# Performance work log

Hardware: AMD Instinct MI355X
Metric: run time of the kernel (lower is better)

## Reference

```python
import jax, jax.numpy as jnp
import numpy as np

B, L, C, H = 2, 2048, 1024, 16  # batches, tokens per batch, channels, heads


def _ln(x, eps=1e-6):
    # LayerNorm32: no affine, eps=1e-6, computed in fp32
    x32 = x.astype(jnp.float32)
    m = x32.mean(-1, keepdims=True)
    v = ((x32 - m) ** 2).mean(-1, keepdims=True)
    return ((x32 - m) * jax.lax.rsqrt(v + eps)).astype(x.dtype)


def setup_inputs() -> dict:
    key = jax.random.key(0)
    ks = jax.random.split(key, 8)
    s = 0.02
    return {
        "feats": jax.random.normal(ks[0], (B * L, C), jnp.float32),
        "mod": jax.random.normal(ks[1], (B, C), jnp.float32),
        "w_mod": jax.random.normal(ks[2], (C, 6 * C), jnp.float32) * s,
        "b_mod": jnp.zeros((6 * C,), jnp.float32),
        "w_qkv": jax.random.normal(ks[3], (C, 3 * C), jnp.float32) * s,
        "b_qkv": jnp.zeros((3 * C,), jnp.float32),
        "w_proj": jax.random.normal(ks[4], (C, C), jnp.float32) * s,
        "b_proj": jnp.zeros((C,), jnp.float32),
        "w_fc1": jax.random.normal(ks[5], (C, 4 * C), jnp.float32) * s,
        "b_fc1": jnp.zeros((4 * C,), jnp.float32),
        "w_fc2": jax.random.normal(ks[6], (4 * C, C), jnp.float32) * s,
        "b_fc2": jnp.zeros((C,), jnp.float32),
        "seq_len": L,
    }


def reference(feats, mod, w_mod, b_mod, w_qkv, b_qkv, w_proj, b_proj,
              w_fc1, b_fc1, w_fc2, b_fc2, seq_len):
    Bn, Cn = mod.shape
    Ln = seq_len
    Hn = H
    D = Cn // Hn

    # adaLN modulation: SiLU -> Linear(C, 6C), chunk into 6 [B, C] pieces
    m = jax.nn.silu(mod) @ w_mod + b_mod
    sh_a, sc_a, g_a, sh_m, sc_m, g_m = jnp.split(m, 6, axis=1)

    x = feats.reshape(Bn, Ln, Cn)

    # --- MSA branch ---
    h = _ln(x)
    h = h * (1.0 + sc_a[:, None]) + sh_a[:, None]
    qkv = h @ w_qkv + b_qkv  # [B, L, 3C]
    q, k, v = [t.reshape(Bn, Ln, Hn, D) for t in jnp.split(qkv, 3, axis=-1)]
    scores = jnp.einsum('bqhd,bkhd->bhqk', q, k) / jnp.sqrt(jnp.float32(D))
    a = jax.nn.softmax(scores, axis=-1)
    o = jnp.einsum('bhqk,bkhd->bqhd', a, v).reshape(Bn, Ln, Cn)
    o = o @ w_proj + b_proj
    x = x + o * g_a[:, None]

    # --- FFN branch ---
    h = _ln(x)
    h = h * (1.0 + sc_m[:, None]) + sh_m[:, None]
    h = jax.nn.gelu(h @ w_fc1 + b_fc1, approximate=False) @ w_fc2 + b_fc2
    x = x + h * g_m[:, None]

    return x.reshape(Bn * Ln, Cn)
```

## Files before the change

### kernel.cpp

```cpp
#include <hip/hip_runtime.h>
#include <hip/hip_bf16.h>
#include <math.h>

#define B_ 2
#define L_ 2048
#define C_ 1024
#define H_ 16
#define D_ 64

typedef __attribute__((ext_vector_type(8))) short short8;
typedef __attribute__((ext_vector_type(4))) float float4v;

__device__ inline short f2bs(float f) {
    union { __hip_bfloat16 h; short s; } u; u.h = __float2bfloat16(f); return u.s;
}

#define GL2LDS(gp, lp)                                                         \
    __builtin_amdgcn_global_load_lds(                                          \
        (const __attribute__((address_space(1))) void*)(gp),                   \
        (__attribute__((address_space(3))) void*)(lp), 16, 0, 0)

__global__ __launch_bounds__(256) void k_mod2(const float* __restrict__ mod,
                                              const float* __restrict__ w_mod,
                                              const float* __restrict__ b_mod,
                                              float* __restrict__ m_out) {
    __shared__ float a_s[2][256];
    const int t = threadIdx.x;
    const int seg = blockIdx.y;
    for (int i = t; i < 512; i += 256) {
        float a = mod[(i >> 8) * C_ + seg * 256 + (i & 255)];
        a_s[i >> 8][i & 255] = a / (1.f + __expf(-a));
    }
    __syncthreads();
    int j = blockIdx.x * 256 + t;
    float acc0 = (seg == 0) ? b_mod[j] : 0.f;
    float acc1 = acc0;
    for (int k = 0; k < 256; ++k) {
        float w = w_mod[(size_t)(seg * 256 + k) * (6 * C_) + j];
        acc0 += a_s[0][k] * w;
        acc1 += a_s[1][k] * w;
    }
    atomicAdd(&m_out[j], acc0);
    atomicAdd(&m_out[6 * C_ + j], acc1);
}

__global__ __launch_bounds__(256) void k_wt_all(
        const float* __restrict__ w_qkv, const float* __restrict__ w_proj,
        const float* __restrict__ w_fc1, const float* __restrict__ w_fc2,
        short* __restrict__ wqkvT, short* __restrict__ wprojT,
        short* __restrict__ wfc1T, short* __restrict__ wfc2T) {
    __shared__ short T[64][72];
    int id = blockIdx.x;
    const float* W; short* WT; int K, N;
    if (id < 768)       {             W = w_qkv;  WT = wqkvT;  K = C_;     N = 3 * C_; }
    else if (id < 1024) { id -= 768;  W = w_proj; WT = wprojT; K = C_;     N = C_;     }
    else if (id < 2048) { id -= 1024; W = w_fc1;  WT = wfc1T;  K = C_;     N = 4 * C_; }
    else                { id -= 2048; W = w_fc2;  WT = wfc2T;  K = 4 * C_; N = C_;     }
    const int nb = N >> 6;
    const int n0 = (id % nb) * 64, k0 = (id / nb) * 64;
    const int t = threadIdx.x;
    {
        int kr = t >> 2, nc = (t & 3) * 16;
        const float* src = W + (size_t)(k0 + kr) * N + n0 + nc;
#pragma unroll
        for (int j = 0; j < 16; ++j) T[kr][nc + j] = f2bs(src[j]);
    }
    __syncthreads();
    {
        int nr = t >> 2, kc = (t & 3) * 16;
        short8 o0, o1;
#pragma unroll
        for (int j = 0; j < 8; ++j) { o0[j] = T[kc + j][nr]; o1[j] = T[kc + 8 + j][nr]; }
        short* dst = WT + (size_t)(n0 + nr) * K + k0 + kc;
        *(short8*)dst = o0;
        *(short8*)(dst + 8) = o1;
    }
}

__global__ __launch_bounds__(256) void k_vt(const __hip_bfloat16* __restrict__ qkv,
                                            short* __restrict__ vt) {
    __shared__ short T[64][72];
    const int t = threadIdx.x;
    const int kt = blockIdx.x * 64;
    const int bh = blockIdx.y;
    const int h = bh & (H_ - 1), b = bh >> 4;
    const __hip_bfloat16* src = qkv + ((size_t)(b * L_ + kt)) * (3 * C_) + 2 * C_ + h * D_;
    {
        int kr = t >> 2, dg = (t & 3) * 16;
        const short8* s = (const short8*)(src + (size_t)kr * (3 * C_) + dg);
        *(short8*)&T[kr][dg] = s[0];
        *(short8*)&T[kr][dg + 8] = s[1];
    }
    __syncthreads();
    {
        int dr = t >> 2, kg = (t & 3) * 16;
        short8 o0, o1;
#pragma unroll
        for (int j = 0; j < 8; ++j) { o0[j] = T[kg + j][dr]; o1[j] = T[kg + 8 + j][dr]; }
        short* dst = vt + ((size_t)bh * D_ + dr) * L_ + kt + kg;
        *(short8*)dst = o0;
        *(short8*)(dst + 8) = o1;
    }
}

__global__ __launch_bounds__(256) void k_ln_mod(const float* __restrict__ x,
                                                const float* __restrict__ mvec,
                                                int off_sh, int off_sc,
                                                __hip_bfloat16* __restrict__ h_out) {
    int row = blockIdx.x;
    int b = row / L_;
    int t = threadIdx.x;
    float v[4];
    float s = 0.f, ss = 0.f;
#pragma unroll
    for (int i = 0; i < 4; ++i) {
        int c = t + i * 256;
        float val = x[(size_t)row * C_ + c];
        v[i] = val; s += val; ss += val * val;
    }
#pragma unroll
    for (int o = 32; o; o >>= 1) { s += __shfl_xor(s, o); ss += __shfl_xor(ss, o); }
    __shared__ float red[2][4];
    int wid = t >> 6, lane = t & 63;
    if (lane == 0) { red[0][wid] = s; red[1][wid] = ss; }
    __syncthreads();
    s  = red[0][0] + red[0][1] + red[0][2] + red[0][3];
    ss = red[1][0] + red[1][1] + red[1][2] + red[1][3];
    float mean = s * (1.f / C_);
    float var  = ss * (1.f / C_) - mean * mean;
    float rstd = rsqrtf(var + 1e-6f);
#pragma unroll
    for (int i = 0; i < 4; ++i) {
        int c = t + i * 256;
        float sc = mvec[b * (6 * C_) + off_sc + c];
        float sh = mvec[b * (6 * C_) + off_sh + c];
        float hn = (v[i] - mean) * rstd;
        h_out[(size_t)row * C_ + c] = __float2bfloat16(hn * (1.f + sc) + sh);
    }
}

__device__ inline void gemm_epilogue(float v, int m, int n, int N, int act, int emode,
                                     const float* __restrict__ gate,
                                     const float* __restrict__ resid_f,
                                     __hip_bfloat16* __restrict__ out_bf,
                                     float* __restrict__ out_f) {
    if (act == 1) v = 0.5f * v * (1.f + erff(v * 0.70710678118654752440f));
    if (emode == 2) {
        float g = gate[(m >> 11) * (6 * C_) + n];
        v = resid_f[(size_t)m * N + n] + v * g;
    }
    if (out_f) out_f[(size_t)m * N + n] = v;
    else       out_bf[(size_t)m * N + n] = __float2bfloat16(v);
}

template<int WM, int WN, int MI, int NI>
__global__ __launch_bounds__(512) void k_gemm_async(
        const __hip_bfloat16* __restrict__ A, int lda,
        const short* __restrict__ WT, int ldw,
        const float* __restrict__ bias,
        int M, int N, int K, int act, int emode,
        const float* __restrict__ gate,
        const float* __restrict__ resid_f,
        __hip_bfloat16* __restrict__ out_bf,
        float* __restrict__ out_f) {
    constexpr int BM = WM * MI * 16;
    constexpr int BN = WN * NI * 16;
    __shared__ __align__(16) short A_lds[2][BM * 64];
    __shared__ __align__(16) short B_lds[2][BN * 64];
    const int t = threadIdx.x;
    const int lane = t & 63;
    const int w = t >> 6;
    const int wm = w / WN, wn = w % WN;
    const int quad = lane >> 4, l16 = lane & 15;

    const int gx = gridDim.x;
    const int nwg = gx * gridDim.y;
    const int lin = blockIdx.y * gx + blockIdx.x;
    const int wg = (lin & 7) * (nwg >> 3) + (lin >> 3);
    const int m0 = (wg / gx) * BM;
    const int n0 = (wg % gx) * BN;

    auto stage = [&](int buf, int k0) {
#pragma unroll
        for (int rep = 0; rep < BM / 64; ++rep) {
            int p = rep * 512 + t;
            int row = p >> 3;
            int g = (p & 7) ^ (row & 7);
            const __hip_bfloat16* gp = A + (size_t)(m0 + row) * lda + k0 + g * 8;
            GL2LDS(gp, &A_lds[buf][(rep * 512 + (t & ~63)) * 8]);
        }
#pragma unroll
        for (int rep = 0; rep < BN / 64; ++rep) {
            int p = rep * 512 + t;
            int row = p >> 3;
            int g = (p & 7) ^ (row & 7);
            const short* gp = WT + (size_t)(n0 + row) * ldw + k0 + g * 8;
            GL2LDS(gp, &B_lds[buf][(rep * 512 + (t & ~63)) * 8]);
        }
    };

    float4v acc[MI][NI] = {};

    stage(0, 0);
    __syncthreads();

    const int nt = K >> 6;
    int cur = 0;
    for (int kt = 0; kt < nt; ++kt) {
        if (kt + 1 < nt) stage(cur ^ 1, (kt + 1) << 6);

        short8 af[MI][2], bfr[NI][2];
#pragma unroll
        for (int mi = 0; mi < MI; ++mi) {
            int r = wm * MI * 16 + mi * 16 + l16;
#pragma unroll
            for (int hh = 0; hh < 2; ++hh)
                af[mi][hh] = *(const short8*)(&A_lds[cur][(r * 8 + ((hh * 4 + quad) ^ (r & 7))) * 8]);
        }
#pragma unroll
        for (int ni = 0; ni < NI; ++ni) {
            int r = wn * NI * 16 + ni * 16 + l16;
#pragma unroll
            for (int hh = 0; hh < 2; ++hh)
                bfr[ni][hh] = *(const short8*)(&B_lds[cur][(r * 8 + ((hh * 4 + quad) ^ (r & 7))) * 8]);
        }
#pragma unroll
        for (int hh = 0; hh < 2; ++hh)
#pragma unroll
            for (int mi = 0; mi < MI; ++mi)
#pragma unroll
                for (int ni = 0; ni < NI; ++ni)
                    acc[mi][ni] = __builtin_amdgcn_mfma_f32_16x16x32_bf16(
                        af[mi][hh], bfr[ni][hh], acc[mi][ni], 0, 0, 0);

        __syncthreads();
        cur ^= 1;
    }

#pragma unroll
    for (int mi = 0; mi < MI; ++mi)
#pragma unroll
        for (int ni = 0; ni < NI; ++ni)
#pragma unroll
            for (int r = 0; r < 4; ++r) {
                int m = m0 + wm * MI * 16 + mi * 16 + quad * 4 + r;
                int n = n0 + wn * NI * 16 + ni * 16 + l16;
                float v = acc[mi][ni][r] + (bias ? bias[n] : 0.f);
                gemm_epilogue(v, m, n, N, act, emode, gate, resid_f, out_bf, out_f);
            }
}

__global__ __launch_bounds__(512) void k_attn(const __hip_bfloat16* __restrict__ qkv,
                                              const short* __restrict__ vt,
                                              __hip_bfloat16* __restrict__ o) {
    __shared__ __align__(16) short K_lds[2][64 * 64];
    __shared__ __align__(16) short V_lds[2][64 * 64];
    __shared__ __align__(16) short P_lds[8][16 * 64];
    const int t = threadIdx.x;
    const int lane = t & 63;
    const int w = t >> 6;
    const int quad = lane >> 4, l16 = lane & 15;

    const int raw = blockIdx.x;
    const int blk = (raw & 7) * 64 + (raw >> 3);
    const int bh = blk >> 4;
    const int q_blk = (blk & 15) * 128;
    const int h = bh & (H_ - 1);
    const int b = bh >> 4;

    const size_t stride = 3 * C_;
    const __hip_bfloat16* base = qkv + (size_t)b * L_ * stride + h * D_;

    short8 qf[2];
    {
        const __hip_bfloat16* qrow = base + (size_t)(q_blk + w * 16 + l16) * stride;
        qf[0] = *(const short8*)(qrow + quad * 8);
        qf[1] = *(const short8*)(qrow + 32 + quad * 8);
    }
    short8 ones;
#pragma unroll
    for (int j = 0; j < 8; ++j) ones[j] = (short)0x3F80;

    const int rx = l16 & 7;
    const int c0 = (quad ^ rx) * 8;
    const int c1 = ((quad + 4) ^ rx) * 8;

    float4v o_acc[4];
    float4v l_acc = (float4v){0.f, 0.f, 0.f, 0.f};
#pragma unroll
    for (int dt = 0; dt < 4; ++dt) o_acc[dt] = (float4v){0.f, 0.f, 0.f, 0.f};

    const int s_row = t >> 3;
    const int s_lc  = t & 7;
    const int s_pc  = s_lc ^ (s_row & 7);
    const __hip_bfloat16* kg = base + C_;
    const short* vtb = vt + (size_t)bh * D_ * L_;

    short8 kreg = *(const short8*)(kg + (size_t)s_row * stride + s_lc * 8);
    short8 vreg = *(const short8*)(vtb + (size_t)s_row * L_ + s_lc * 8);
    *(short8*)&K_lds[0][s_row * 64 + s_pc * 8] = kreg;
    *(short8*)&V_lds[0][s_row * 64 + s_pc * 8] = vreg;
    __syncthreads();

    for (int kt = 0, cur = 0; kt < L_; kt += 64, cur ^= 1) {
        const int nxt = kt + 64;
        if (nxt < L_) {
            kreg = *(const short8*)(kg + (size_t)(nxt + s_row) * stride + s_lc * 8);
            vreg = *(const short8*)(vtb + (size_t)s_row * L_ + nxt + s_lc * 8);
        }

        float4v sacc[4];
        __builtin_amdgcn_s_setprio(1);
#pragma unroll
        for (int kb = 0; kb < 4; ++kb) {
            sacc[kb] = (float4v){0.f, 0.f, 0.f, 0.f};
            short8 kf0 = *(const short8*)(&K_lds[cur][(kb * 16 + l16) * 64 + c0]);
            short8 kf1 = *(const short8*)(&K_lds[cur][(kb * 16 + l16) * 64 + c1]);
            sacc[kb] = __builtin_amdgcn_mfma_f32_16x16x32_bf16(qf[0], kf0, sacc[kb], 0, 0, 0);
            sacc[kb] = __builtin_amdgcn_mfma_f32_16x16x32_bf16(qf[1], kf1, sacc[kb], 0, 0, 0);
        }
        __builtin_amdgcn_s_setprio(0);

        {
            const int ci = l16 >> 3, wi = l16 & 7;
#pragma unroll
            for (int r = 0; r < 4; ++r) {
                const int prow_i = quad * 4 + r;
                const int rw = prow_i & 7;
                short* prow = &P_lds[w][prow_i * 64];
                prow[((0 + ci) ^ rw) * 8 + wi] = f2bs(__expf(fmaf(sacc[0][r], 0.125f, -8.f)));
                prow[((2 + ci) ^ rw) * 8 + wi] = f2bs(__expf(fmaf(sacc[1][r], 0.125f, -8.f)));
                prow[((4 + ci) ^ rw) * 8 + wi] = f2bs(__expf(fmaf(sacc[2][r], 0.125f, -8.f)));
                prow[((6 + ci) ^ rw) * 8 + wi] = f2bs(__expf(fmaf(sacc[3][r], 0.125f, -8.f)));
            }
        }

        short8 pf0 = *(const short8*)(&P_lds[w][l16 * 64 + c0]);
        short8 pf1 = *(const short8*)(&P_lds[w][l16 * 64 + c1]);
        __builtin_amdgcn_s_setprio(1);
        l_acc = __builtin_amdgcn_mfma_f32_16x16x32_bf16(pf0, ones, l_acc, 0, 0, 0);
        l_acc = __builtin_amdgcn_mfma_f32_16x16x32_bf16(pf1, ones, l_acc, 0, 0, 0);
#pragma unroll
        for (int dt = 0; dt < 4; ++dt) {
            short8 vf0 = *(const short8*)(&V_lds[cur][(dt * 16 + l16) * 64 + c0]);
            short8 vf1 = *(const short8*)(&V_lds[cur][(dt * 16 + l16) * 64 + c1]);
            o_acc[dt] = __builtin_amdgcn_mfma_f32_16x16x32_bf16(pf0, vf0, o_acc[dt], 0, 0, 0);
            o_acc[dt] = __builtin_amdgcn_mfma_f32_16x16x32_bf16(pf1, vf1, o_acc[dt], 0, 0, 0);
        }
        __builtin_amdgcn_s_setprio(0);

        if (nxt < L_) {
            *(short8*)&K_lds[cur ^ 1][s_row * 64 + s_pc * 8] = kreg;
            *(short8*)&V_lds[cur ^ 1][s_row * 64 + s_pc * 8] = vreg;
        }
        __syncthreads();
    }

#pragma unroll
    for (int dt = 0; dt < 4; ++dt)
#pragma unroll
        for (int r = 0; r < 4; ++r) {
            int q = q_blk + w * 16 + quad * 4 + r;
            o[(size_t)(b * L_ + q) * C_ + h * D_ + dt * 16 + l16] =
                __float2bfloat16(o_acc[dt][r] / l_acc[r]);
        }
}

extern "C" void kernel_launch(void* const* d_in, const int* in_sizes, int n_in,
                              void* d_out, int out_size, void* d_ws, size_t ws_size,
                              hipStream_t stream) {
    const float* feats  = (const float*)d_in[0];
    const float* mod    = (const float*)d_in[1];
    const float* w_mod  = (const float*)d_in[2];
    const float* b_mod  = (const float*)d_in[3];
    const float* w_qkv  = (const float*)d_in[4];
    const float* b_qkv  = (const float*)d_in[5];
    const float* w_proj = (const float*)d_in[6];
    const float* b_proj = (const float*)d_in[7];
    const float* w_fc1  = (const float*)d_in[8];
    const float* b_fc1  = (const float*)d_in[9];
    const float* w_fc2  = (const float*)d_in[10];
    const float* b_fc2  = (const float*)d_in[11];

    const int M = B_ * L_;
    char* ws = (char*)d_ws;
    float* m_ws = (float*)ws;

    short* wqkvT  = (short*)(ws + 49152);
    short* wprojT = wqkvT + (size_t)3 * C_ * C_;
    short* wfc1T  = wprojT + (size_t)C_ * C_;
    short* wfc2T  = wfc1T + (size_t)4 * C_ * C_;
    char* slotB = (char*)(wfc2T + (size_t)4 * C_ * C_);
    __hip_bfloat16* qkv_ws = (__hip_bfloat16*)slotB;
    float* x1_ws           = (float*)slotB;
    __hip_bfloat16* slotA  = (__hip_bfloat16*)(slotB + (size_t)M * 3 * C_ * 2);
    __hip_bfloat16* hf_ws  = slotA + (size_t)M * C_;
    short* vt_ws           = (short*)hf_ws;

    k_wt_all<<<3072, 256, 0, stream>>>(w_qkv, w_proj, w_fc1, w_fc2,
                                       wqkvT, wprojT, wfc1T, wfc2T);
    hipMemsetAsync(m_ws, 0, 2 * 6 * C_ * sizeof(float), stream);
    k_mod2<<<dim3(24, 4), 256, 0, stream>>>(mod, w_mod, b_mod, m_ws);
    k_ln_mod<<<M, 256, 0, stream>>>(feats, m_ws, 0, 1024, slotA);
    k_gemm_async<2, 4, 4, 2><<<dim3(3 * C_ / 128, M / 128), 512, 0, stream>>>(
        slotA, C_, wqkvT, C_, b_qkv, M, 3 * C_, C_, 0, 0,
        nullptr, nullptr, qkv_ws, nullptr);
    k_vt<<<dim3(L_ / 64, B_ * H_), 256, 0, stream>>>(qkv_ws, vt_ws);
    k_attn<<<B_ * H_ * (L_ / 128), 512, 0, stream>>>(qkv_ws, vt_ws, slotA);
    k_gemm_async<4, 2, 2, 2><<<dim3(C_ / 64, M / 128), 512, 0, stream>>>(
        slotA, C_, wprojT, C_, b_proj, M, C_, C_, 0, 2,
        m_ws + 2 * C_, feats, nullptr, x1_ws);
    k_ln_mod<<<M, 256, 0, stream>>>(x1_ws, m_ws, 3 * C_, 4 * C_, slotA);
    k_gemm_async<2, 4, 4, 2><<<dim3(4 * C_ / 128, M / 128), 512, 0, stream>>>(
        slotA, C_, wfc1T, C_, b_fc1, M, 4 * C_, C_, 1, 0,
        nullptr, nullptr, hf_ws, nullptr);
    k_gemm_async<4, 2, 2, 2><<<dim3(C_ / 64, M / 128), 512, 0, stream>>>(
        hf_ws, 4 * C_, wfc2T, 4 * C_, b_fc2, M, C_, 4 * C_, 0, 2,
        m_ws + 5 * C_, x1_ws, nullptr, (float*)d_out);
}
```

Measured before the change: 433.8 us.

## Add 256x256 8-wave GEMM with interleaved LDS staging for QKV and FC1

```diff
diff --git a/kernel.cpp b/kernel.cpp
--- a/kernel.cpp
+++ b/kernel.cpp
@@ -19,6 +19,12 @@
     __builtin_amdgcn_global_load_lds(                                          \
         (const __attribute__((address_space(1))) void*)(gp),                   \
         (__attribute__((address_space(3))) void*)(lp), 16, 0, 0)
+
+#define SBAR() do { __builtin_amdgcn_sched_barrier(0);                         \
+                    __builtin_amdgcn_s_barrier();                              \
+                    __builtin_amdgcn_sched_barrier(0); } while (0)
+#define LGKM0() do { asm volatile("s_waitcnt lgkmcnt(0)" ::: "memory");        \
+                     __builtin_amdgcn_sched_barrier(0); } while (0)
 
 __global__ __launch_bounds__(256) void k_mod2(const float* __restrict__ mod,
                                               const float* __restrict__ w_mod,
@@ -151,6 +157,124 @@
     }
     if (out_f) out_f[(size_t)m * N + n] = v;
     else       out_bf[(size_t)m * N + n] = __float2bfloat16(v);
+}
+
+__global__ __launch_bounds__(512) void k_gemm8(
+        const __hip_bfloat16* __restrict__ A, int lda,
+        const short* __restrict__ WT, int ldw,
+        const float* __restrict__ bias,
+        int M, int N, int K, int act, int emode,
+        const float* __restrict__ gate,
+        const float* __restrict__ resid_f,
+        __hip_bfloat16* __restrict__ out_bf,
+        float* __restrict__ out_f) {
+    __shared__ __align__(16) short A_lds[2][2][256 * 32];
+    __shared__ __align__(16) short B_lds[2][2][256 * 32];
+    const int t = threadIdx.x;
+    const int lane = t & 63;
+    const int w = t >> 6;
+    const int wm = w >> 2, wn = w & 3;
+    const int quad = lane >> 4, l16 = lane & 15;
+
+    const int gx = gridDim.x;
+    const int nwg = gx * gridDim.y;
+    const int lin = blockIdx.y * gx + blockIdx.x;
+    const int wg = (lin & 7) * (nwg >> 3) + (lin >> 3);
+    const int m0 = (wg / gx) * 256;
+    const int n0 = (wg % gx) * 256;
+
+    const int sr  = t >> 2;
+    const int sck = (t & 3) * 8;
+    const int sdw = (t & ~63) * 8;
+
+    auto stageA = [&](int buf, int kb, int kh) {
+        const __hip_bfloat16* g0 = A + (size_t)(m0 + sr) * lda + kb + kh * 32 + sck;
+        const __hip_bfloat16* g1 = A + (size_t)(m0 + sr + 128) * lda + kb + kh * 32 + sck;
+        GL2LDS(g0, &A_lds[buf][kh][sdw]);
+        GL2LDS(g1, &A_lds[buf][kh][sdw + 4096]);
+    };
+    auto stageB = [&](int buf, int kb, int kh) {
+        const short* g0 = WT + (size_t)(n0 + sr) * ldw + kb + kh * 32 + sck;
+        const short* g1 = WT + (size_t)(n0 + sr + 128) * ldw + kb + kh * 32 + sck;
+        GL2LDS(g0, &B_lds[buf][kh][sdw]);
+        GL2LDS(g1, &B_lds[buf][kh][sdw + 4096]);
+    };
+
+    float4v acc[8][4] = {};
+    short8 fA[4], fB[4];
+    const int nt = K >> 6;
+
+    stageB(0, 0, 0);  stageA(0, 0, 0);  stageB(0, 0, 1);  stageA(0, 0, 1);
+    stageB(1, 64, 0); stageA(1, 64, 0); stageB(1, 64, 1);
+    asm volatile("s_waitcnt vmcnt(6)" ::: "memory");
+    SBAR();
+
+#define RD_A(kh, mg)                                                           \
+    _Pragma("unroll")                                                          \
+    for (int mi = 0; mi < 4; ++mi)                                             \
+        fA[mi] = *(const short8*)(&A_lds[cur][kh][(wm * 128 + (mg) * 64 + mi * 16 + l16) * 32 + quad * 8]);
+#define RD_B(kh)                                                               \
+    _Pragma("unroll")                                                          \
+    for (int ni = 0; ni < 4; ++ni)                                             \
+        fB[ni] = *(const short8*)(&B_lds[cur][kh][(wn * 64 + ni * 16 + l16) * 32 + quad * 8]);
+#define DO_MFMA(mg)                                                            \
+    __builtin_amdgcn_s_setprio(1);                                             \
+    _Pragma("unroll")                                                          \
+    for (int mi = 0; mi < 4; ++mi)                                             \
+        _Pragma("unroll")                                                      \
+        for (int ni = 0; ni < 4; ++ni)                                         \
+            acc[(mg) * 4 + mi][ni] = __builtin_amdgcn_mfma_f32_16x16x32_bf16(  \
+                fA[mi], fB[ni], acc[(mg) * 4 + mi][ni], 0, 0, 0);              \
+    __builtin_amdgcn_s_setprio(0);
+
+    for (int kt = 0; kt < nt; ++kt) {
+        const int cur = kt & 1;
+        const int kb1 = (kt + 1) << 6;
+        const int kb2 = (kt + 2) << 6;
+
+        RD_A(0, 0); RD_B(0);
+        if (kt + 1 < nt) stageA(cur ^ 1, kb1, 1);
+        SBAR(); LGKM0();
+        DO_MFMA(0);
+        SBAR();
+
+        RD_A(0, 1);
+        if (kt + 2 < nt) stageB(cur, kb2, 0);
+        SBAR(); LGKM0();
+        DO_MFMA(1);
+        SBAR();
+
+        RD_A(1, 0); RD_B(1);
+        if (kt + 2 < nt) stageA(cur, kb2, 0);
+        SBAR(); LGKM0();
+        DO_MFMA(0);
+        SBAR();
+
+        RD_A(1, 1);
+        if (kt + 2 < nt) stageB(cur, kb2, 1);
+        SBAR(); LGKM0();
+        DO_MFMA(1);
+        if (kt + 1 < nt) {
+            if (kt + 2 < nt) asm volatile("s_waitcnt vmcnt(6)" ::: "memory");
+            else             asm volatile("s_waitcnt vmcnt(0)" ::: "memory");
+        }
+        SBAR();
+    }
+#undef RD_A
+#undef RD_B
+#undef DO_MFMA
+
+#pragma unroll
+    for (int a = 0; a < 8; ++a)
+#pragma unroll
+        for (int ni = 0; ni < 4; ++ni)
+#pragma unroll
+            for (int r = 0; r < 4; ++r) {
+                int m = m0 + wm * 128 + (a >> 2) * 64 + (a & 3) * 16 + quad * 4 + r;
+                int n = n0 + wn * 64 + ni * 16 + l16;
+                float v = acc[a][ni][r] + (bias ? bias[n] : 0.f);
+                gemm_epilogue(v, m, n, N, act, emode, gate, resid_f, out_bf, out_f);
+            }
 }
 
 template<int WM, int WN, int MI, int NI>
@@ -402,7 +526,7 @@
     hipMemsetAsync(m_ws, 0, 2 * 6 * C_ * sizeof(float), stream);
     k_mod2<<<dim3(24, 4), 256, 0, stream>>>(mod, w_mod, b_mod, m_ws);
     k_ln_mod<<<M, 256, 0, stream>>>(feats, m_ws, 0, 1024, slotA);
-    k_gemm_async<2, 4, 4, 2><<<dim3(3 * C_ / 128, M / 128), 512, 0, stream>>>(
+    k_gemm8<<<dim3(3 * C_ / 256, M / 256), 512, 0, stream>>>(
         slotA, C_, wqkvT, C_, b_qkv, M, 3 * C_, C_, 0, 0,
         nullptr, nullptr, qkv_ws, nullptr);
     k_vt<<<dim3(L_ / 64, B_ * H_), 256, 0, stream>>>(qkv_ws, vt_ws);
@@ -411,7 +535,7 @@
         slotA, C_, wprojT, C_, b_proj, M, C_, C_, 0, 2,
         m_ws + 2 * C_, feats, nullptr, x1_ws);
     k_ln_mod<<<M, 256, 0, stream>>>(x1_ws, m_ws, 3 * C_, 4 * C_, slotA);
-    k_gemm_async<2, 4, 4, 2><<<dim3(4 * C_ / 128, M / 128), 512, 0, stream>>>(
+    k_gemm8<<<dim3(4 * C_ / 256, M / 256), 512, 0, stream>>>(
         slotA, C_, wfc1T, C_, b_fc1, M, 4 * C_, C_, 1, 0,
         nullptr, nullptr, hf_ws, nullptr);
     k_gemm_async<4, 2, 2, 2><<<dim3(C_ / 64, M / 128), 512, 0, stream>>>(
```

New measurement: 461.1 us. 6.3% more time.
